# Performance work log

Measured on AMD Instinct MI355X. Metric: run time of the kernel, lower is better.

Reference implementation:

```python
import jax, jax.numpy as jnp
import numpy as np

EPS = 1e-15
PROJ_EPS = 1e-05


def project_hyp_vec(x):
    # clamp squared norm from below at 1 - PROJ_EPS (torch.clamp with min only)
    norm = jnp.sum(x * x, axis=-1, keepdims=True)
    return x * (1.0 - PROJ_EPS) / jnp.maximum(norm, 1.0 - PROJ_EPS)


def atanh(x):
    return 0.5 * jnp.log((1.0 + x) / (1.0 - x))


def mob_add(u, v):
    v = v + EPS
    norm_uv = 2.0 * jnp.sum(u * v, axis=-1, keepdims=True)
    norm_u = jnp.sum(u * u, axis=-1, keepdims=True)
    norm_v = jnp.sum(v * v, axis=-1, keepdims=True)
    denom = 1.0 + norm_uv + norm_v * norm_u
    result = (1.0 + norm_uv + norm_v) / denom * u + (1.0 - norm_u) / denom * v
    return project_hyp_vec(result)


def mob_mat_mul(M, x):
    x = project_hyp_vec(x)
    Mx = x @ M                                   # [B, H]
    Mx_norm = jnp.linalg.norm(Mx + EPS, axis=-1, keepdims=True)
    x_norm = jnp.linalg.norm(x + EPS, axis=-1, keepdims=True)
    return project_hyp_vec(jnp.tanh(Mx_norm / x_norm * atanh(x_norm)) / Mx_norm * Mx)


def setup_inputs() -> dict:
    key = jax.random.key(0)
    k_in, k_w, k_u = jax.random.split(key, 3)
    B, S, I, H = 256, 512, 256, 256
    inputs = jax.random.normal(k_in, (B, S, I), dtype=jnp.float32) * 0.1
    k = (1.0 / H) ** 0.5
    w = jax.random.uniform(k_w, (H, H), minval=-k, maxval=k, dtype=jnp.float32)
    u = jax.random.uniform(k_u, (I, H), minval=-k, maxval=k, dtype=jnp.float32)
    b = jnp.zeros((H,), dtype=jnp.float32)
    return {"inputs": inputs, "w": w, "u": u, "b": b}


def reference(inputs, w, u, b):
    B, S, I = inputs.shape
    H = w.shape[0]

    def step(h, x):
        Wh = mob_mat_mul(w, h)          # [B, H]
        Ux = mob_mat_mul(u, x)          # [B, H]
        h_new = mob_add(mob_add(Wh, Ux), b)
        return h_new, h_new

    h0 = jnp.zeros((B, H), dtype=inputs.dtype)
    _, outs = jax.lax.scan(step, h0, jnp.swapaxes(inputs, 0, 1))  # [S, B, H]
    return jnp.swapaxes(outs, 0, 1)  # [B, S, H]
```

## Files before the change

kernel.cpp:

```cpp
#include <hip/hip_runtime.h>

#define EPSV 1e-15f
#define PEPS 1e-5f

typedef float v2f __attribute__((ext_vector_type(2)));

__device__ __forceinline__ float frcp(float x) { return __builtin_amdgcn_rcpf(x); }
__device__ __forceinline__ float fexp2(float x) { return __builtin_amdgcn_exp2f(x); }
__device__ __forceinline__ float flog2(float x) { return __builtin_amdgcn_logf(x); }
__device__ __forceinline__ float projscale(float n2) {
  return n2 > (1.f - PEPS) ? (1.f - PEPS) * frcp(n2) : 1.f;
}

template <int CTRL>
__device__ __forceinline__ float dppadd(float x) {
  int y = __builtin_amdgcn_update_dpp(0, __float_as_int(x), CTRL, 0xF, 0xF, true);
  return x + __int_as_float(y);
}
__device__ __forceinline__ float wave_sum(float x) {
  x = dppadd<0x111>(x);
  x = dppadd<0x112>(x);
  x = dppadd<0x114>(x);
  x = dppadd<0x118>(x);
  x = dppadd<0x142>(x);
  x = dppadd<0x143>(x);
  return __int_as_float(__builtin_amdgcn_readlane(__float_as_int(x), 63));
}

__global__ __launch_bounds__(256) void ux_kernel(
    const float* __restrict__ x, const float* __restrict__ u,
    const float* __restrict__ bvec, float* __restrict__ out,
    float4* __restrict__ vstat, int use_vstat)
{
  __shared__ __align__(16) float xsT[256][36];

  const int tid = threadIdx.x;
  const int lane = tid & 63, wv = tid >> 6;
  const long long base = (long long)blockIdx.x * 32;

  #pragma unroll
  for (int k4 = 0; k4 < 8; ++k4) {
    float t0 = x[(base + k4 * 4 + 0) * 256 + tid];
    float t1 = x[(base + k4 * 4 + 1) * 256 + tid];
    float t2 = x[(base + k4 * 4 + 2) * 256 + tid];
    float t3 = x[(base + k4 * 4 + 3) * 256 + tid];
    float4 v; v.x = t0; v.y = t1; v.z = t2; v.w = t3;
    *reinterpret_cast<float4*>(&xsT[tid][k4 * 4]) = v;
  }
  __syncthreads();

  float4 bb = *reinterpret_cast<const float4*>(&bvec[4 * lane]);
  bb.x += EPSV; bb.y += EPSV; bb.z += EPSV; bb.w += EPSV;
  float S_vbrow = wave_sum(bb.x + bb.y + bb.z + bb.w);

  float s1[8], s2[8];
  #pragma unroll
  for (int r = 0; r < 8; ++r) { s1[r] = 0.f; s2[r] = 0.f; }
  #pragma unroll
  for (int c = 0; c < 4; ++c) {
    const int i = lane + 64 * c;
    float4 xa = *reinterpret_cast<const float4*>(&xsT[i][8 * wv]);
    float4 xb = *reinterpret_cast<const float4*>(&xsT[i][8 * wv + 4]);
    s1[0] += xa.x; s2[0] += xa.x * xa.x;
    s1[1] += xa.y; s2[1] += xa.y * xa.y;
    s1[2] += xa.z; s2[2] += xa.z * xa.z;
    s1[3] += xa.w; s2[3] += xa.w * xa.w;
    s1[4] += xb.x; s2[4] += xb.x * xb.x;
    s1[5] += xb.y; s2[5] += xb.y * xb.y;
    s1[6] += xb.z; s2[6] += xb.z * xb.z;
    s1[7] += xb.w; s2[7] += xb.w * xb.w;
  }
  float rs[8], xnr[8];
  #pragma unroll
  for (int r = 0; r < 8; ++r) {
    float a = wave_sum(s1[r]);
    float b2 = wave_sum(s2[r]);
    float sc = projscale(b2);
    rs[r] = sc;
    xnr[r] = sqrtf(sc * sc * b2 + 2.f * sc * EPSV * a + 256.f * EPSV * EPSV);
  }

  float4 acc[8];
  #pragma unroll
  for (int r = 0; r < 8; ++r) { acc[r].x = 0.f; acc[r].y = 0.f; acc[r].z = 0.f; acc[r].w = 0.f; }
  #pragma unroll 2
  for (int i = 0; i < 256; ++i) {
    float4 uv = *reinterpret_cast<const float4*>(&u[i * 256 + 4 * lane]);
    float4 xa = *reinterpret_cast<const float4*>(&xsT[i][8 * wv]);
    float4 xb = *reinterpret_cast<const float4*>(&xsT[i][8 * wv + 4]);
    acc[0].x += uv.x * xa.x; acc[0].y += uv.y * xa.x; acc[0].z += uv.z * xa.x; acc[0].w += uv.w * xa.x;
    acc[1].x += uv.x * xa.y; acc[1].y += uv.y * xa.y; acc[1].z += uv.z * xa.y; acc[1].w += uv.w * xa.y;
    acc[2].x += uv.x * xa.z; acc[2].y += uv.y * xa.z; acc[2].z += uv.z * xa.z; acc[2].w += uv.w * xa.z;
    acc[3].x += uv.x * xa.w; acc[3].y += uv.y * xa.w; acc[3].z += uv.z * xa.w; acc[3].w += uv.w * xa.w;
    acc[4].x += uv.x * xb.x; acc[4].y += uv.y * xb.x; acc[4].z += uv.z * xb.x; acc[4].w += uv.w * xb.x;
    acc[5].x += uv.x * xb.y; acc[5].y += uv.y * xb.y; acc[5].z += uv.z * xb.y; acc[5].w += uv.w * xb.y;
    acc[6].x += uv.x * xb.z; acc[6].y += uv.y * xb.z; acc[6].z += uv.z * xb.z; acc[6].w += uv.w * xb.z;
    acc[7].x += uv.x * xb.w; acc[7].y += uv.y * xb.w; acc[7].z += uv.z * xb.w; acc[7].w += uv.w * xb.w;
  }

  #pragma unroll
  for (int r = 0; r < 8; ++r) {
    float t1 = wave_sum(acc[r].x + acc[r].y + acc[r].z + acc[r].w);
    float t2 = wave_sum(acc[r].x * acc[r].x + acc[r].y * acc[r].y +
                        acc[r].z * acc[r].z + acc[r].w * acc[r].w);
    float t3 = wave_sum(acc[r].x * bb.x + acc[r].y * bb.y + acc[r].z * bb.z + acc[r].w * bb.w);
    float Sm  = rs[r] * t1;
    float Sm2 = rs[r] * rs[r] * t2;
    float mxn = sqrtf(Sm2 + 2.f * EPSV * Sm + 256.f * EPSV * EPSV);
    float xn = xnr[r];
    float at = 0.34657359f * flog2((1.f + xn) * frcp(1.f - xn));
    float arg = mxn * frcp(xn) * at;
    float e2 = fexp2(arg * 2.8853902f);
    float th = 1.f - 2.f * frcp(e2 + 1.f);
    float g = th * frcp(mxn);
    float fs = g * projscale(g * g * Sm2) * rs[r];
    float4 o;
    o.x = fs * acc[r].x + EPSV; o.y = fs * acc[r].y + EPSV;
    o.z = fs * acc[r].z + EPSV; o.w = fs * acc[r].w + EPSV;
    reinterpret_cast<float4*>(out)[(base + 8 * wv + r) * 64 + lane] = o;
    if (use_vstat && lane == 0) {
      float Sv  = fs * t1 + 256.f * EPSV;
      float Sv2 = fs * fs * t2 + 2.f * EPSV * fs * t1 + 256.f * EPSV * EPSV;
      float Svb = fs * t3 + EPSV * S_vbrow;
      vstat[base + 8 * wv + r] = float4{Sv, Sv2, Svb, 0.f};
    }
  }
}

template <int NR>
__device__ __forceinline__ void load_w(const float* __restrict__ w, int rb, int lane, v2f* wr) {
  #pragma unroll
  for (int r = 0; r < NR; ++r) {
    float4 t = *reinterpret_cast<const float4*>(&w[(rb + r) * 256 + 4 * lane]);
    asm volatile("" : "+v"(t.x), "+v"(t.y), "+v"(t.z), "+v"(t.w));
    wr[2 * r]     = v2f{t.x, t.y};
    wr[2 * r + 1] = v2f{t.z, t.w};
  }
}

template <int NR>
__device__ __forceinline__ void mv_pq(const v2f* wr, const float* mxp, const float* vp,
                                      float4& P, float4& Q) {
  v2f pl{0.f, 0.f}, ph{0.f, 0.f}, ql{0.f, 0.f}, qh{0.f, 0.f};
  #pragma unroll
  for (int i = 0; i < NR / 4; ++i) {
    float4 h4 = *reinterpret_cast<const float4*>(mxp + 4 * i);
    float4 u4 = *reinterpret_cast<const float4*>(vp + 4 * i);
    pl += wr[8 * i + 0] * h4.x; ph += wr[8 * i + 1] * h4.x;
    pl += wr[8 * i + 2] * h4.y; ph += wr[8 * i + 3] * h4.y;
    pl += wr[8 * i + 4] * h4.z; ph += wr[8 * i + 5] * h4.z;
    pl += wr[8 * i + 6] * h4.w; ph += wr[8 * i + 7] * h4.w;
    ql += wr[8 * i + 0] * u4.x; qh += wr[8 * i + 1] * u4.x;
    ql += wr[8 * i + 2] * u4.y; qh += wr[8 * i + 3] * u4.y;
    ql += wr[8 * i + 4] * u4.z; qh += wr[8 * i + 5] * u4.z;
    ql += wr[8 * i + 6] * u4.w; qh += wr[8 * i + 7] * u4.w;
  }
  P = float4{pl.x, pl.y, ph.x, ph.y};
  Q = float4{ql.x, ql.y, qh.x, qh.y};
}

__device__ __forceinline__ int row_base(int wv) {
  if (wv == 0) return 0;
  if (wv <= 13) return 8 + (wv - 1) * 16;
  return 216 + (wv - 14) * 20;
}

__global__ __launch_bounds__(1024)
__attribute__((amdgpu_waves_per_eu(4, 4)))
void rnn_kernel(
    const float* __restrict__ w, const float* __restrict__ bvec,
    float* __restrict__ out, const float4* __restrict__ vstat, int S, int use_vstat)
{
  __shared__ __align__(16) float mx_lds[256];
  __shared__ __align__(16) float v_lds[2][256];
  __shared__ __align__(16) float pP[16][256];
  __shared__ __align__(16) float pQ[16][256];

  const int tid = threadIdx.x;
  const int lane = tid & 63;
  const int wv = tid >> 6;

  const long long rb4 = (long long)blockIdx.x * S * 64;
  const long long vsbase = (long long)blockIdx.x * S;
  const float4* outv = reinterpret_cast<const float4*>(out);
  float4* outw = reinterpret_cast<float4*>(out);
  const float4 zero4{0.f, 0.f, 0.f, 0.f};

  if (wv == 0) {
    v2f wr[16];
    load_w<8>(w, 0, lane, wr);

    float4 vb4 = *reinterpret_cast<const float4*>(&bvec[4 * lane]);
    vb4.x += EPSV; vb4.y += EPSV; vb4.z += EPSV; vb4.w += EPSV;
    float S_vb  = wave_sum(vb4.x + vb4.y + vb4.z + vb4.w);
    float S_vb2 = wave_sum(vb4.x * vb4.x + vb4.y * vb4.y + vb4.z * vb4.z + vb4.w * vb4.w);

    reinterpret_cast<float4*>(mx_lds)[lane] = zero4;
    reinterpret_cast<float4*>(v_lds[0])[lane] = vb4;
    __syncthreads();

    {
      float4 P, Q; mv_pq<8>(wr, &mx_lds[0], &v_lds[0][0], P, Q);
      *reinterpret_cast<float4*>(&pP[0][4 * lane]) = P;
      *reinterpret_cast<float4*>(&pQ[0][4 * lane]) = Q;
    }
    __syncthreads();

    float4 Wvb4 = zero4;
    #pragma unroll
    for (int k = 0; k < 16; ++k) {
      float4 qq = *reinterpret_cast<const float4*>(&pQ[k][4 * lane]);
      Wvb4.x += qq.x; Wvb4.y += qq.y; Wvb4.z += qq.z; Wvb4.w += qq.w;
    }
    float sAx = 0.f, sAy = 0.f, sAz = 0.f;
    if (use_vstat) { float4 s = vstat[vsbase]; sAx = s.x; sAy = s.y; sAz = s.z; }
    __syncthreads();

    float4 m4 = zero4;
    float S_h = 0.f, S_h2 = 0.f;

    for (int t = 0; t < S; ++t) {
      const int b = t & 1;
      float nsx = 0.f, nsy = 0.f, nsz = 0.f;
      if (use_vstat && t + 1 < S) { float4 s = vstat[vsbase + t + 1]; nsx = s.x; nsy = s.y; nsz = s.z; }

      float4 v4 = *reinterpret_cast<const float4*>(&v_lds[b][4 * lane]);

      float S_Mx  = wave_sum(m4.x + m4.y + m4.z + m4.w);
      float S_Mx2 = wave_sum(m4.x * m4.x + m4.y * m4.y + m4.z * m4.z + m4.w * m4.w);
      float S_Mxv = wave_sum(m4.x * v4.x + m4.y * v4.y + m4.z * v4.z + m4.w * v4.w);
      float S_Mxb = wave_sum(m4.x * vb4.x + m4.y * vb4.y + m4.z * vb4.z + m4.w * vb4.w);
      float S_v, S_v2, S_vvb;
      if (use_vstat) { S_v = sAx; S_v2 = sAy; S_vvb = sAz; }
      else {
        S_v   = wave_sum(v4.x + v4.y + v4.z + v4.w);
        S_v2  = wave_sum(v4.x * v4.x + v4.y * v4.y + v4.z * v4.z + v4.w * v4.w);
        S_vvb = wave_sum(v4.x * vb4.x + v4.y * vb4.y + v4.z * vb4.z + v4.w * vb4.w);
      }

      float s_hp = projscale(S_h2);
      float xn = sqrtf(s_hp * s_hp * S_h2 + 2.f * s_hp * EPSV * S_h + 256.f * EPSV * EPSV);
      float mxn = sqrtf(S_Mx2 + 2.f * EPSV * S_Mx + 256.f * EPSV * EPSV);
      float at = 0.34657359f * flog2((1.f + xn) * frcp(1.f - xn));
      float arg = mxn * frcp(xn) * at;
      float e2 = fexp2(arg * 2.8853902f);
      float th = 1.f - 2.f * frcp(e2 + 1.f);
      float g = th * frcp(mxn);
      float beta = g * projscale(g * g * S_Mx2);

      float nuv = 2.f * beta * S_Mxv;
      float nu  = beta * beta * S_Mx2;
      float nv  = S_v2;
      float rden = frcp(1.f + nuv + nv * nu);
      float cA = (1.f + nuv + nv) * rden;
      float cB = (1.f - nu) * rden;
      float cAb = cA * beta;
      float S_r1  = cAb * S_Mx + cB * S_v;
      float S_r12 = cAb * cAb * S_Mx2 + 2.f * cAb * cB * S_Mxv + cB * cB * S_v2;
      float S_r1b = cAb * S_Mxb + cB * S_vvb;
      float s1p = projscale(S_r12);
      float S_U = s1p * S_r1, S_U2 = s1p * s1p * S_r12, S_Ub = s1p * S_r1b;

      float nuv2 = 2.f * S_Ub;
      float rden2 = frcp(1.f + nuv2 + S_vb2 * S_U2);
      float dA = (1.f + nuv2 + S_vb2) * rden2;
      float dB = (1.f - S_U2) * rden2;
      float S_hn  = dA * S_U + dB * S_vb;
      float S_hn2 = dA * dA * S_U2 + 2.f * dA * dB * S_Ub + dB * dB * S_vb2;
      float s2p = projscale(S_hn2);

      float km = s2p * dA * s1p * cAb;
      float kv = s2p * dA * s1p * cB;
      float kb = s2p * dB;

      float4 hn{km * m4.x + kv * v4.x + kb * vb4.x,
                km * m4.y + kv * v4.y + kb * vb4.y,
                km * m4.z + kv * v4.z + kb * vb4.z,
                km * m4.w + kv * v4.w + kb * vb4.w};
      outw[rb4 + (long long)t * 64 + lane] = hn;

      S_h  = s2p * S_hn;
      S_h2 = s2p * s2p * S_hn2;
      float snextp = projscale(S_h2);

      {
        float4 P, Q; mv_pq<8>(wr, &mx_lds[0], &v_lds[b][0], P, Q);
        *reinterpret_cast<float4*>(&pP[0][4 * lane]) = P;
        *reinterpret_cast<float4*>(&pQ[0][4 * lane]) = Q;
      }
      __syncthreads();

      float4 Pc = zero4, Qc = zero4;
      #pragma unroll
      for (int k = 0; k < 16; ++k) {
        float4 pp = *reinterpret_cast<const float4*>(&pP[k][4 * lane]);
        float4 qq = *reinterpret_cast<const float4*>(&pQ[k][4 * lane]);
        Pc.x += pp.x; Pc.y += pp.y; Pc.z += pp.z; Pc.w += pp.w;
        Qc.x += qq.x; Qc.y += qq.y; Qc.z += qq.z; Qc.w += qq.w;
      }
      m4.x = snextp * (km * Pc.x + kv * Qc.x + kb * Wvb4.x);
      m4.y = snextp * (km * Pc.y + kv * Qc.y + kb * Wvb4.y);
      m4.z = snextp * (km * Pc.z + kv * Qc.z + kb * Wvb4.z);
      m4.w = snextp * (km * Pc.w + kv * Qc.w + kb * Wvb4.w);
      reinterpret_cast<float4*>(mx_lds)[lane] = m4;
      __syncthreads();

      sAx = nsx; sAy = nsy; sAz = nsz;
    }
  } else if (wv == 1) {
    v2f wr[32];
    const int rb = row_base(1);
    load_w<16>(w, rb, lane, wr);

    float4 vA = outv[rb4 + lane];
    float4 vB = outv[rb4 + 64 + lane];
    float4 vC = outv[rb4 + 128 + lane];
    __syncthreads();
    {
      float4 P, Q; mv_pq<16>(wr, &mx_lds[rb], &v_lds[0][rb], P, Q);
      *reinterpret_cast<float4*>(&pP[1][4 * lane]) = P;
      *reinterpret_cast<float4*>(&pQ[1][4 * lane]) = Q;
    }
    __syncthreads();
    reinterpret_cast<float4*>(v_lds[0])[lane] = vA;
    __syncthreads();

    for (int t = 0; t < S; ++t) {
      const int b = t & 1;
      float4 P, Q;
      mv_pq<16>(wr, &mx_lds[rb], &v_lds[b][rb], P, Q);
      *reinterpret_cast<float4*>(&pP[1][4 * lane]) = P;
      *reinterpret_cast<float4*>(&pQ[1][4 * lane]) = Q;
      if (t + 1 < S) reinterpret_cast<float4*>(v_lds[(t + 1) & 1])[lane] = vB;
      vB = vC;
      if (t + 3 < S) vC = outv[rb4 + (long long)(t + 3) * 64 + lane];
      __syncthreads();
      __syncthreads();
    }
  } else {
    const int rb = row_base(wv);
    if (wv >= 14) {
      v2f wr[40];
      load_w<20>(w, rb, lane, wr);
      __syncthreads();
      {
        float4 P, Q; mv_pq<20>(wr, &mx_lds[rb], &v_lds[0][rb], P, Q);
        *reinterpret_cast<float4*>(&pP[wv][4 * lane]) = P;
        *reinterpret_cast<float4*>(&pQ[wv][4 * lane]) = Q;
      }
      __syncthreads();
      __syncthreads();
      for (int t = 0; t < S; ++t) {
        const int b = t & 1;
        float4 P, Q;
        mv_pq<20>(wr, &mx_lds[rb], &v_lds[b][rb], P, Q);
        *reinterpret_cast<float4*>(&pP[wv][4 * lane]) = P;
        *reinterpret_cast<float4*>(&pQ[wv][4 * lane]) = Q;
        __syncthreads();
        __syncthreads();
      }
    } else {
      v2f wr[32];
      load_w<16>(w, rb, lane, wr);
      __syncthreads();
      {
        float4 P, Q; mv_pq<16>(wr, &mx_lds[rb], &v_lds[0][rb], P, Q);
        *reinterpret_cast<float4*>(&pP[wv][4 * lane]) = P;
        *reinterpret_cast<float4*>(&pQ[wv][4 * lane]) = Q;
      }
      __syncthreads();
      __syncthreads();
      for (int t = 0; t < S; ++t) {
        const int b = t & 1;
        float4 P, Q;
        mv_pq<16>(wr, &mx_lds[rb], &v_lds[b][rb], P, Q);
        *reinterpret_cast<float4*>(&pP[wv][4 * lane]) = P;
        *reinterpret_cast<float4*>(&pQ[wv][4 * lane]) = Q;
        __syncthreads();
        __syncthreads();
      }
    }
  }
}

extern "C" void kernel_launch(void* const* d_in, const int* in_sizes, int n_in,
                              void* d_out, int out_size, void* d_ws, size_t ws_size,
                              hipStream_t stream) {
  const float* x = (const float*)d_in[0];
  const float* w = (const float*)d_in[1];
  const float* u = (const float*)d_in[2];
  const float* b = (const float*)d_in[3];
  float* out = (float*)d_out;

  const int nrows = in_sizes[0] / 256;
  const int S = 512;
  const int B = nrows / S;

  const int use_vstat = (ws_size >= (size_t)nrows * 16) ? 1 : 0;
  float4* vstat = (float4*)d_ws;

  ux_kernel<<<nrows / 32, 256, 0, stream>>>(x, u, b, out, vstat, use_vstat);
  rnn_kernel<<<B, 1024, 0, stream>>>(w, b, out, vstat, S, use_vstat);
}
```

Baseline: 963.7 us.

## Split W matvec between LDS-resident rows and registers, offload reduction to helper waves

Copies the first 112 rows of W into LDS. Waves 2-15 now compute the matvec partials, using 8 LDS rows plus 8 or 12 register rows each, so waves 0 and 1 hold no W and do no matvec work. Reducing the partial sums and writing the new Mx is moved from wave 0 to waves 1, 13, 14 and 15, which each handle 64 columns. The scalar coefficients are passed through LDS. This is meant to cut register pressure and shorten the serial critical path on wave 0. In exchange it adds LDS traffic for W on every step and a scalar round-trip through LDS.

```diff
diff --git a/kernel.cpp b/kernel.cpp
--- a/kernel.cpp
+++ b/kernel.cpp
@@ -138,43 +138,56 @@
   }
 }
 
-template <int NR>
-__device__ __forceinline__ void mv_pq(const v2f* wr, const float* mxp, const float* vp,
-                                      float4& P, float4& Q) {
-  v2f pl{0.f, 0.f}, ph{0.f, 0.f}, ql{0.f, 0.f}, qh{0.f, 0.f};
-  #pragma unroll
-  for (int i = 0; i < NR / 4; ++i) {
-    float4 h4 = *reinterpret_cast<const float4*>(mxp + 4 * i);
-    float4 u4 = *reinterpret_cast<const float4*>(vp + 4 * i);
-    pl += wr[8 * i + 0] * h4.x; ph += wr[8 * i + 1] * h4.x;
-    pl += wr[8 * i + 2] * h4.y; ph += wr[8 * i + 3] * h4.y;
-    pl += wr[8 * i + 4] * h4.z; ph += wr[8 * i + 5] * h4.z;
-    pl += wr[8 * i + 6] * h4.w; ph += wr[8 * i + 7] * h4.w;
-    ql += wr[8 * i + 0] * u4.x; qh += wr[8 * i + 1] * u4.x;
-    ql += wr[8 * i + 2] * u4.y; qh += wr[8 * i + 3] * u4.y;
-    ql += wr[8 * i + 4] * u4.z; qh += wr[8 * i + 5] * u4.z;
-    ql += wr[8 * i + 6] * u4.w; qh += wr[8 * i + 7] * u4.w;
-  }
-  P = float4{pl.x, pl.y, ph.x, ph.y};
-  Q = float4{ql.x, ql.y, qh.x, qh.y};
-}
-
-__device__ __forceinline__ int row_base(int wv) {
-  if (wv == 0) return 0;
-  if (wv <= 13) return 8 + (wv - 1) * 16;
-  return 216 + (wv - 14) * 20;
-}
-
-__global__ __launch_bounds__(1024)
-__attribute__((amdgpu_waves_per_eu(4, 4)))
-void rnn_kernel(
+#define NLDSROW 112
+
+template <int NREG>
+__device__ __forceinline__ void mv_step(const float (*Wl)[256], const v2f* wr,
+                                        int ldsb, int regb, int lane,
+                                        const float* mxp, const float* vp,
+                                        float* pPrw, float* pQrw) {
+  v2f pl{0.f,0.f}, ph{0.f,0.f}, ql{0.f,0.f}, qh{0.f,0.f};
+  #pragma unroll
+  for (int i = 0; i < 2; ++i) {
+    float4 h4 = *reinterpret_cast<const float4*>(mxp + ldsb + 4 * i);
+    float4 u4 = *reinterpret_cast<const float4*>(vp + ldsb + 4 * i);
+    float hh[4] = {h4.x, h4.y, h4.z, h4.w};
+    float uu[4] = {u4.x, u4.y, u4.z, u4.w};
+    #pragma unroll
+    for (int j = 0; j < 4; ++j) {
+      float4 w4 = *reinterpret_cast<const float4*>(&Wl[ldsb + 4 * i + j][4 * lane]);
+      v2f wl{w4.x, w4.y}, wh{w4.z, w4.w};
+      pl += wl * hh[j]; ph += wh * hh[j];
+      ql += wl * uu[j]; qh += wh * uu[j];
+    }
+  }
+  #pragma unroll
+  for (int i = 0; i < NREG / 4; ++i) {
+    float4 h4 = *reinterpret_cast<const float4*>(mxp + regb + 4 * i);
+    float4 u4 = *reinterpret_cast<const float4*>(vp + regb + 4 * i);
+    float hh[4] = {h4.x, h4.y, h4.z, h4.w};
+    float uu[4] = {u4.x, u4.y, u4.z, u4.w};
+    #pragma unroll
+    for (int j = 0; j < 4; ++j) {
+      v2f wl = wr[8 * i + 2 * j], wh = wr[8 * i + 2 * j + 1];
+      pl += wl * hh[j]; ph += wh * hh[j];
+      ql += wl * uu[j]; qh += wh * uu[j];
+    }
+  }
+  *reinterpret_cast<float4*>(pPrw + 4 * lane) = float4{pl.x, pl.y, ph.x, ph.y};
+  *reinterpret_cast<float4*>(pQrw + 4 * lane) = float4{ql.x, ql.y, qh.x, qh.y};
+}
+
+__global__ __launch_bounds__(1024) void rnn_kernel(
     const float* __restrict__ w, const float* __restrict__ bvec,
     float* __restrict__ out, const float4* __restrict__ vstat, int S, int use_vstat)
 {
+  __shared__ __align__(16) float W_lds[NLDSROW][256];
   __shared__ __align__(16) float mx_lds[256];
   __shared__ __align__(16) float v_lds[2][256];
+  __shared__ __align__(16) float wvb_lds[256];
   __shared__ __align__(16) float pP[16][256];
   __shared__ __align__(16) float pQ[16][256];
+  __shared__ float sc_lds[4];
 
   const int tid = threadIdx.x;
   const int lane = tid & 63;
@@ -186,10 +199,17 @@
   float4* outw = reinterpret_cast<float4*>(out);
   const float4 zero4{0.f, 0.f, 0.f, 0.f};
 
+  {
+    const float4* w4 = reinterpret_cast<const float4*>(w);
+    float4* wl4 = reinterpret_cast<float4*>(&W_lds[0][0]);
+    #pragma unroll
+    for (int c = 0; c < 7; ++c) {
+      int idx = c * 1024 + tid;
+      wl4[idx] = w4[idx];
+    }
+  }
+
   if (wv == 0) {
-    v2f wr[16];
-    load_w<8>(w, 0, lane, wr);
-
     float4 vb4 = *reinterpret_cast<const float4*>(&bvec[4 * lane]);
     vb4.x += EPSV; vb4.y += EPSV; vb4.z += EPSV; vb4.w += EPSV;
     float S_vb  = wave_sum(vb4.x + vb4.y + vb4.z + vb4.w);
@@ -198,33 +218,21 @@
     reinterpret_cast<float4*>(mx_lds)[lane] = zero4;
     reinterpret_cast<float4*>(v_lds[0])[lane] = vb4;
     __syncthreads();
-
-    {
-      float4 P, Q; mv_pq<8>(wr, &mx_lds[0], &v_lds[0][0], P, Q);
-      *reinterpret_cast<float4*>(&pP[0][4 * lane]) = P;
-      *reinterpret_cast<float4*>(&pQ[0][4 * lane]) = Q;
-    }
-    __syncthreads();
-
-    float4 Wvb4 = zero4;
-    #pragma unroll
-    for (int k = 0; k < 16; ++k) {
-      float4 qq = *reinterpret_cast<const float4*>(&pQ[k][4 * lane]);
-      Wvb4.x += qq.x; Wvb4.y += qq.y; Wvb4.z += qq.z; Wvb4.w += qq.w;
-    }
+    __syncthreads();
+
     float sAx = 0.f, sAy = 0.f, sAz = 0.f;
     if (use_vstat) { float4 s = vstat[vsbase]; sAx = s.x; sAy = s.y; sAz = s.z; }
     __syncthreads();
 
-    float4 m4 = zero4;
     float S_h = 0.f, S_h2 = 0.f;
 
     for (int t = 0; t < S; ++t) {
       const int b = t & 1;
+      float4 m4 = *reinterpret_cast<const float4*>(&mx_lds[4 * lane]);
+      float4 v4 = *reinterpret_cast<const float4*>(&v_lds[b][4 * lane]);
+
       float nsx = 0.f, nsy = 0.f, nsz = 0.f;
       if (use_vstat && t + 1 < S) { float4 s = vstat[vsbase + t + 1]; nsx = s.x; nsy = s.y; nsz = s.z; }
-
-      float4 v4 = *reinterpret_cast<const float4*>(&v_lds[b][4 * lane]);
 
       float S_Mx  = wave_sum(m4.x + m4.y + m4.z + m4.w);
       float S_Mx2 = wave_sum(m4.x * m4.x + m4.y * m4.y + m4.z * m4.z + m4.w * m4.w);
@@ -283,102 +291,92 @@
       S_h2 = s2p * s2p * S_hn2;
       float snextp = projscale(S_h2);
 
-      {
-        float4 P, Q; mv_pq<8>(wr, &mx_lds[0], &v_lds[b][0], P, Q);
-        *reinterpret_cast<float4*>(&pP[0][4 * lane]) = P;
-        *reinterpret_cast<float4*>(&pQ[0][4 * lane]) = Q;
+      if (lane == 0) {
+        sc_lds[0] = snextp * km;
+        sc_lds[1] = snextp * kv;
+        sc_lds[2] = snextp * kb;
       }
-      __syncthreads();
-
-      float4 Pc = zero4, Qc = zero4;
-      #pragma unroll
-      for (int k = 0; k < 16; ++k) {
-        float4 pp = *reinterpret_cast<const float4*>(&pP[k][4 * lane]);
-        float4 qq = *reinterpret_cast<const float4*>(&pQ[k][4 * lane]);
-        Pc.x += pp.x; Pc.y += pp.y; Pc.z += pp.z; Pc.w += pp.w;
-        Qc.x += qq.x; Qc.y += qq.y; Qc.z += qq.z; Qc.w += qq.w;
-      }
-      m4.x = snextp * (km * Pc.x + kv * Qc.x + kb * Wvb4.x);
-      m4.y = snextp * (km * Pc.y + kv * Qc.y + kb * Wvb4.y);
-      m4.z = snextp * (km * Pc.z + kv * Qc.z + kb * Wvb4.z);
-      m4.w = snextp * (km * Pc.w + kv * Qc.w + kb * Wvb4.w);
-      reinterpret_cast<float4*>(mx_lds)[lane] = m4;
+
+      __syncthreads();
       __syncthreads();
 
       sAx = nsx; sAy = nsy; sAz = nsz;
     }
   } else if (wv == 1) {
-    v2f wr[32];
-    const int rb = row_base(1);
-    load_w<16>(w, rb, lane, wr);
-
     float4 vA = outv[rb4 + lane];
     float4 vB = outv[rb4 + 64 + lane];
     float4 vC = outv[rb4 + 128 + lane];
     __syncthreads();
+    __syncthreads();
     {
-      float4 P, Q; mv_pq<16>(wr, &mx_lds[rb], &v_lds[0][rb], P, Q);
-      *reinterpret_cast<float4*>(&pP[1][4 * lane]) = P;
-      *reinterpret_cast<float4*>(&pQ[1][4 * lane]) = Q;
-    }
-    __syncthreads();
-    reinterpret_cast<float4*>(v_lds[0])[lane] = vA;
+      const int c = lane;
+      float qc = 0.f;
+      #pragma unroll
+      for (int k = 2; k < 16; ++k) qc += pQ[k][c];
+      wvb_lds[c] = qc;
+      reinterpret_cast<float4*>(v_lds[0])[lane] = vA;
+    }
     __syncthreads();
 
     for (int t = 0; t < S; ++t) {
-      const int b = t & 1;
-      float4 P, Q;
-      mv_pq<16>(wr, &mx_lds[rb], &v_lds[b][rb], P, Q);
-      *reinterpret_cast<float4*>(&pP[1][4 * lane]) = P;
-      *reinterpret_cast<float4*>(&pQ[1][4 * lane]) = Q;
       if (t + 1 < S) reinterpret_cast<float4*>(v_lds[(t + 1) & 1])[lane] = vB;
       vB = vC;
       if (t + 3 < S) vC = outv[rb4 + (long long)(t + 3) * 64 + lane];
       __syncthreads();
+      {
+        const int c = lane;
+        float s0 = sc_lds[0], s1 = sc_lds[1], s2 = sc_lds[2];
+        float pc = 0.f, qc = 0.f;
+        #pragma unroll
+        for (int k = 2; k < 16; ++k) { pc += pP[k][c]; qc += pQ[k][c]; }
+        mx_lds[c] = s0 * pc + s1 * qc + s2 * wvb_lds[c];
+      }
+      __syncthreads();
+    }
+  } else if (wv <= 9) {
+    const int ldsb = 8 * (wv - 2);
+    const int regb = 112 + 12 * (wv - 2);
+    v2f wr[24];
+    load_w<12>(w, regb, lane, wr);
+    __syncthreads();
+    mv_step<12>(W_lds, wr, ldsb, regb, lane, mx_lds, v_lds[0], pP[wv], pQ[wv]);
+    __syncthreads();
+    __syncthreads();
+    for (int t = 0; t < S; ++t) {
+      const int b = t & 1;
+      mv_step<12>(W_lds, wr, ldsb, regb, lane, mx_lds, v_lds[b], pP[wv], pQ[wv]);
+      __syncthreads();
       __syncthreads();
     }
   } else {
-    const int rb = row_base(wv);
-    if (wv >= 14) {
-      v2f wr[40];
-      load_w<20>(w, rb, lane, wr);
-      __syncthreads();
-      {
-        float4 P, Q; mv_pq<20>(wr, &mx_lds[rb], &v_lds[0][rb], P, Q);
-        *reinterpret_cast<float4*>(&pP[wv][4 * lane]) = P;
-        *reinterpret_cast<float4*>(&pQ[wv][4 * lane]) = Q;
+    const int ldsb = 8 * (wv - 2);
+    const int regb = 208 + 8 * (wv - 10);
+    const bool docmb = (wv >= 13);
+    const int c = 64 * (wv - 12) + lane;
+    v2f wr[16];
+    load_w<8>(w, regb, lane, wr);
+    __syncthreads();
+    mv_step<8>(W_lds, wr, ldsb, regb, lane, mx_lds, v_lds[0], pP[wv], pQ[wv]);
+    __syncthreads();
+    if (docmb) {
+      float qc = 0.f;
+      #pragma unroll
+      for (int k = 2; k < 16; ++k) qc += pQ[k][c];
+      wvb_lds[c] = qc;
+    }
+    __syncthreads();
+    for (int t = 0; t < S; ++t) {
+      const int b = t & 1;
+      mv_step<8>(W_lds, wr, ldsb, regb, lane, mx_lds, v_lds[b], pP[wv], pQ[wv]);
+      __syncthreads();
+      if (docmb) {
+        float s0 = sc_lds[0], s1 = sc_lds[1], s2 = sc_lds[2];
+        float pc = 0.f, qc = 0.f;
+        #pragma unroll
+        for (int k = 2; k < 16; ++k) { pc += pP[k][c]; qc += pQ[k][c]; }
+        mx_lds[c] = s0 * pc + s1 * qc + s2 * wvb_lds[c];
       }
       __syncthreads();
-      __syncthreads();
-      for (int t = 0; t < S; ++t) {
-        const int b = t & 1;
-        float4 P, Q;
-        mv_pq<20>(wr, &mx_lds[rb], &v_lds[b][rb], P, Q);
-        *reinterpret_cast<float4*>(&pP[wv][4 * lane]) = P;
-        *reinterpret_cast<float4*>(&pQ[wv][4 * lane]) = Q;
-        __syncthreads();
-        __syncthreads();
-      }
-    } else {
-      v2f wr[32];
-      load_w<16>(w, rb, lane, wr);
-      __syncthreads();
-      {
-        float4 P, Q; mv_pq<16>(wr, &mx_lds[rb], &v_lds[0][rb], P, Q);
-        *reinterpret_cast<float4*>(&pP[wv][4 * lane]) = P;
-        *reinterpret_cast<float4*>(&pQ[wv][4 * lane]) = Q;
-      }
-      __syncthreads();
-      __syncthreads();
-      for (int t = 0; t < S; ++t) {
-        const int b = t & 1;
-        float4 P, Q;
-        mv_pq<16>(wr, &mx_lds[rb], &v_lds[b][rb], P, Q);
-        *reinterpret_cast<float4*>(&pP[wv][4 * lane]) = P;
-        *reinterpret_cast<float4*>(&pQ[wv][4 * lane]) = Q;
-        __syncthreads();
-        __syncthreads();
-      }
     }
   }
 }
```

After: 911.7 us. -5.4%, faster.
